# Performance work log

Measured on AMD Instinct MI355X. Metric: run time of the kernel, lower is better.

## Reference

```python
import jax, jax.numpy as jnp
import numpy as np

D_MODEL = 1024
NUM_HEADS = 16
HEAD_SIZE = D_MODEL // NUM_HEADS
ROPE_BASE = 10000.0
RMS_EPS = 1e-6


def rms_norm(x, scale):
    # torchtune RMSNorm: fp32 compute, eps=1e-6, learned scale
    xf = x.astype(jnp.float32)
    n = xf * jax.lax.rsqrt(jnp.mean(xf * xf, axis=-1, keepdims=True) + RMS_EPS)
    return (n * scale).astype(x.dtype)


def rope(x):
    # torchtune RotaryPositionalEmbeddings: interleaved pairs. x: [B,T,H,hd]
    B, T, H, hd = x.shape
    half = hd // 2
    theta = 1.0 / (ROPE_BASE ** (jnp.arange(0, hd, 2, dtype=jnp.float32) / hd))  # [half]
    ang = jnp.arange(T, dtype=jnp.float32)[:, None] * theta[None, :]  # [T,half]
    cos = jnp.cos(ang)[None, :, None, :]  # [1,T,1,half]
    sin = jnp.sin(ang)[None, :, None, :]
    xs = x.reshape(B, T, H, half, 2)
    x0, x1 = xs[..., 0], xs[..., 1]
    out = jnp.stack([x0 * cos - x1 * sin, x1 * cos + x0 * sin], axis=-1)
    return out.reshape(B, T, H, hd).astype(x.dtype)


def setup_inputs() -> dict:
    key = jax.random.key(0)
    ks = jax.random.split(key, 10)
    s = 0.02
    D = D_MODEL
    return {
        "x": jax.random.normal(ks[0], (2, 2048, D), dtype=jnp.float32),
        "rms_scale": jnp.ones((D,), dtype=jnp.float32),
        "in_proj_w": jax.random.normal(ks[1], (3 * D, D), dtype=jnp.float32) * s,
        "in_proj_b": jnp.zeros((3 * D,), dtype=jnp.float32),
        "out_proj_w": jax.random.normal(ks[2], (D, D), dtype=jnp.float32) * s,
        "out_proj_b": jnp.zeros((D,), dtype=jnp.float32),
        "w1": jax.random.normal(ks[3], (4 * D, D), dtype=jnp.float32) * s,
        "b1": jnp.zeros((4 * D,), dtype=jnp.float32),
        "w2": jax.random.normal(ks[4], (D, 4 * D), dtype=jnp.float32) * s,
        "b2": jnp.zeros((D,), dtype=jnp.float32),
    }


def reference(x, rms_scale, in_proj_w, in_proj_b, out_proj_w, out_proj_b, w1, b1, w2, b2):
    B, T, D = x.shape
    H, hd = NUM_HEADS, HEAD_SIZE

    xn = rms_norm(x, rms_scale)
    # RoPE on pre-projection q/k (as in original module), value = xn
    q_in = rope(xn.reshape(B, T, H, hd)).reshape(B, T, D)
    k_in = rope(xn.reshape(B, T, H, hd)).reshape(B, T, D)
    v_in = xn

    Wq, Wk, Wv = jnp.split(in_proj_w, 3, axis=0)
    bq, bk, bv = jnp.split(in_proj_b, 3, axis=0)
    q = (q_in @ Wq.T + bq).reshape(B, T, H, hd).transpose(0, 2, 1, 3)  # [B,H,T,hd]
    k = (k_in @ Wk.T + bk).reshape(B, T, H, hd).transpose(0, 2, 1, 3)
    v = (v_in @ Wv.T + bv).reshape(B, T, H, hd).transpose(0, 2, 1, 3)

    scores = jnp.einsum('bhqd,bhkd->bhqk', q, k) / jnp.sqrt(jnp.float32(hd))
    causal = jnp.tril(jnp.ones((T, T), dtype=bool))  # True = keep
    scores = jnp.where(causal[None, None], scores, jnp.float32(-1e30))
    attn = jax.nn.softmax(scores, axis=-1)
    ctx = jnp.einsum('bhqk,bhkd->bhqd', attn, v)  # [B,H,T,hd]
    attn_out = ctx.transpose(0, 2, 1, 3).reshape(B, T, D) @ out_proj_w.T + out_proj_b

    # NOTE: original overwrites x with attention output (no residual on attention)
    y = attn_out
    yn = rms_norm(y, rms_scale)
    ffn = jax.nn.silu(yn @ w1.T + b1) @ w2.T + b2
    return y + ffn
```

## Files before the change

kernel.cpp:

```cpp
#include <hip/hip_runtime.h>
#include <math.h>
#include <stdint.h>

#define D_MODEL 1024
#define NUM_HEADS 16
#define HEAD_SIZE 64
#define SEQ_T 2048

typedef __bf16 bf16;
typedef __bf16 bf16x8 __attribute__((ext_vector_type(8)));
typedef float f32x4 __attribute__((ext_vector_type(4)));

__device__ __forceinline__ void gld_lds16(const bf16* g, bf16* l) {
    __builtin_amdgcn_global_load_lds(
        (__attribute__((address_space(1))) void*)(const_cast<bf16*>(g)),
        (__attribute__((address_space(3))) void*)(l), 16, 0, 0);
}

struct __align__(8) b4pack { bf16 v[4]; };

__global__ __launch_bounds__(256) void cast_all_weights(const float* __restrict__ s0, bf16* __restrict__ d0, int n0,
                                                        const float* __restrict__ s1, bf16* __restrict__ d1, int n1,
                                                        const float* __restrict__ s2, bf16* __restrict__ d2, int n2,
                                                        const float* __restrict__ s3, bf16* __restrict__ d3, int n3) {
    int i = (blockIdx.x * 256 + threadIdx.x) * 4;
    const float* src;
    bf16* dst;
    if (i < n0) { src = s0; dst = d0; }
    else if (i < n0 + n1) { i -= n0; src = s1; dst = d1; }
    else if (i < n0 + n1 + n2) { i -= n0 + n1; src = s2; dst = d2; }
    else { i -= n0 + n1 + n2; if (i >= n3) return; src = s3; dst = d3; }
    float4 v = *(const float4*)(src + i);
    b4pack o;
    o.v[0] = (bf16)v.x; o.v[1] = (bf16)v.y; o.v[2] = (bf16)v.z; o.v[3] = (bf16)v.w;
    *(b4pack*)(dst + i) = o;
}

__global__ __launch_bounds__(256) void rmsnorm_rope_kernel(const float* __restrict__ x,
                                                           const float* __restrict__ scale,
                                                           bf16* __restrict__ xn,
                                                           bf16* __restrict__ rp, int T) {
    __shared__ float red[4];
    int row = blockIdx.x;
    int t = row % T;
    const float* xp = x + (size_t)row * D_MODEL;
    int tid = threadIdx.x;
    float4 xv = *(const float4*)(xp + tid * 4);
    float s = xv.x * xv.x + xv.y * xv.y + xv.z * xv.z + xv.w * xv.w;
    for (int off = 32; off; off >>= 1) s += __shfl_down(s, off);
    if ((tid & 63) == 0) red[tid >> 6] = s;
    __syncthreads();
    if (tid == 0) red[0] = red[0] + red[1] + red[2] + red[3];
    __syncthreads();
    float inv = rsqrtf(red[0] * (1.0f / D_MODEL) + 1e-6f);
    float4 sc = *(const float4*)(scale + tid * 4);
    float n0 = xv.x * inv * sc.x, n1 = xv.y * inv * sc.y;
    float n2 = xv.z * inv * sc.z, n3 = xv.w * inv * sc.w;
    b4pack pn;
    pn.v[0] = (bf16)n0; pn.v[1] = (bf16)n1; pn.v[2] = (bf16)n2; pn.v[3] = (bf16)n3;
    *(b4pack*)(xn + (size_t)row * D_MODEL + tid * 4) = pn;
    int p0 = 2 * tid;
    float th0 = expf(-0.2878231366242557f * (float)(p0 & 31));
    float th1 = expf(-0.2878231366242557f * (float)((p0 + 1) & 31));
    float s0, c0, s1, c1;
    sincosf((float)t * th0, &s0, &c0);
    sincosf((float)t * th1, &s1, &c1);
    b4pack pr;
    pr.v[0] = (bf16)(n0 * c0 - n1 * s0);
    pr.v[1] = (bf16)(n1 * c0 + n0 * s0);
    pr.v[2] = (bf16)(n2 * c1 - n3 * s1);
    pr.v[3] = (bf16)(n3 * c1 + n2 * s1);
    *(b4pack*)(rp + (size_t)row * D_MODEL + tid * 4) = pr;
}

__global__ __launch_bounds__(256) void rmsnorm_kernel(const float* __restrict__ x,
                                                      const float* __restrict__ scale,
                                                      bf16* __restrict__ out) {
    __shared__ float red[4];
    int row = blockIdx.x;
    const float* xp = x + (size_t)row * D_MODEL;
    bf16* op = out + (size_t)row * D_MODEL;
    int tid = threadIdx.x;
    float s = 0.f;
    for (int i = tid; i < D_MODEL; i += 256) { float v = xp[i]; s += v * v; }
    for (int off = 32; off; off >>= 1) s += __shfl_down(s, off);
    if ((tid & 63) == 0) red[tid >> 6] = s;
    __syncthreads();
    if (tid == 0) red[0] = red[0] + red[1] + red[2] + red[3];
    __syncthreads();
    float inv = rsqrtf(red[0] * (1.0f / D_MODEL) + 1e-6f);
    for (int i = tid; i < D_MODEL; i += 256) op[i] = (bf16)(xp[i] * inv * scale[i]);
}

template <int ACT, int ADD, int OUT_BF16, int VT>
__global__ __launch_bounds__(256) void gemm_bf16(const bf16* __restrict__ A,
                                                 const bf16* __restrict__ A2, int splitN,
                                                 const bf16* __restrict__ W,
                                                 const float* __restrict__ bias,
                                                 float* __restrict__ Cf,
                                                 bf16* __restrict__ Cb,
                                                 bf16* __restrict__ Vtp, int Tlen,
                                                 int M, int N, int K) {
    __shared__ __align__(16) bf16 As[128 * 32];
    __shared__ __align__(16) bf16 Bs[128 * 32];
    int tid = threadIdx.x;
    int m0 = blockIdx.y * 128, n0 = blockIdx.x * 128;
    const bf16* Ag = (n0 < splitN) ? A : A2;

    int lane = tid & 63, w = tid >> 6;
    int wm = w >> 1, wn = w & 1;
    int lm = lane & 15, quad = lane >> 4;

    int c0 = tid, c1 = tid + 256;
    int ar0 = c0 >> 2, ak0 = (c0 & 3) * 8;
    int ar1 = c1 >> 2, ak1 = (c1 & 3) * 8;

    f32x4 acc[4][4];
#pragma unroll
    for (int i = 0; i < 4; i++)
#pragma unroll
        for (int j = 0; j < 4; j++)
#pragma unroll
            for (int r = 0; r < 4; r++) acc[i][j][r] = 0.f;

    int abase = (wm * 64 + lm) * 32 + quad * 8;
    int bbase = (wn * 64 + lm) * 32 + quad * 8;

    for (int k0 = 0; k0 < K; k0 += 32) {
        __syncthreads();
        gld_lds16(Ag + (size_t)(m0 + ar0) * K + k0 + ak0, As + c0 * 8);
        gld_lds16(Ag + (size_t)(m0 + ar1) * K + k0 + ak1, As + c1 * 8);
        gld_lds16(W  + (size_t)(n0 + ar0) * K + k0 + ak0, Bs + c0 * 8);
        gld_lds16(W  + (size_t)(n0 + ar1) * K + k0 + ak1, Bs + c1 * 8);
        __syncthreads();
        bf16x8 af[4], bfr[4];
#pragma unroll
        for (int i = 0; i < 4; i++) af[i] = *(const bf16x8*)&As[abase + i * 16 * 32];
#pragma unroll
        for (int j = 0; j < 4; j++) bfr[j] = *(const bf16x8*)&Bs[bbase + j * 16 * 32];
#pragma unroll
        for (int i = 0; i < 4; i++)
#pragma unroll
            for (int j = 0; j < 4; j++)
                acc[i][j] = __builtin_amdgcn_mfma_f32_16x16x32_bf16(af[i], bfr[j], acc[i][j], 0, 0, 0);
    }

    if (VT && n0 >= 2 * D_MODEL) {
#pragma unroll
        for (int j = 0; j < 4; j++) {
            int col = n0 + wn * 64 + j * 16 + lm;
            int dimg = col - 2 * D_MODEL;
            float bv = bias[col];
#pragma unroll
            for (int i = 0; i < 4; i++) {
                int row0 = m0 + wm * 64 + i * 16 + quad * 4;
                int bb = row0 / Tlen, t0 = row0 % Tlen;
                b4pack pk;
#pragma unroll
                for (int r = 0; r < 4; r++) pk.v[r] = (bf16)(acc[i][j][r] + bv);
                *(b4pack*)(Vtp + ((size_t)bb * D_MODEL + dimg) * Tlen + t0) = pk;
            }
        }
        return;
    }

#pragma unroll
    for (int j = 0; j < 4; j++) {
        int col = n0 + wn * 64 + j * 16 + lm;
        float bv = bias[col];
#pragma unroll
        for (int i = 0; i < 4; i++) {
#pragma unroll
            for (int r = 0; r < 4; r++) {
                int row = m0 + wm * 64 + i * 16 + quad * 4 + r;
                float v = acc[i][j][r] + bv;
                if (ACT == 1) v = v / (1.f + __expf(-v));
                size_t idx = (size_t)row * N + col;
                if (ADD) v += Cf[idx];
                if (OUT_BF16) Cb[idx] = (bf16)v;
                else Cf[idx] = v;
            }
        }
    }
}

template <int ADD>
__global__ __launch_bounds__(256) void gemm_bf16_skinny2(const bf16* __restrict__ A,
                                                         const bf16* __restrict__ W,
                                                         const float* __restrict__ bias,
                                                         float* __restrict__ Cf,
                                                         int M, int N, int K) {
    __shared__ __align__(16) bf16 As[2][64 * 64];
    __shared__ __align__(16) bf16 Bs[2][128 * 64];
    int tid = threadIdx.x;

    int nblk = gridDim.x;
    int q = nblk >> 3;
    int swz = (blockIdx.x & 7) * q + (blockIdx.x >> 3);
    int nb = swz & 7;
    int mb = swz >> 3;
    int m0 = mb * 64, n0 = nb * 128;

    int lane = tid & 63, w = tid >> 6;
    int wm = w >> 1, wn = w & 1;
    int lm = lane & 15, quad = lane >> 4;
    int lm7 = lm & 7;

    int ar0 = tid >> 3, ac0 = (tid & 7) ^ (ar0 & 7);
    int t1 = tid + 256;
    int ar1 = t1 >> 3, ac1 = (t1 & 7) ^ (ar1 & 7);

    f32x4 acc[2][4];
#pragma unroll
    for (int i = 0; i < 2; i++)
#pragma unroll
        for (int j = 0; j < 4; j++)
#pragma unroll
            for (int r = 0; r < 4; r++) acc[i][j][r] = 0.f;

    int nt = K >> 6;

    {
        gld_lds16(A + (size_t)(m0 + ar0) * K + ac0 * 8, &As[0][0] + tid * 8);
        gld_lds16(A + (size_t)(m0 + ar1) * K + ac1 * 8, &As[0][0] + t1 * 8);
#pragma unroll
        for (int i = 0; i < 4; i++) {
            int c = tid + 256 * i;
            int r = c >> 3, cc = (c & 7) ^ (r & 7);
            gld_lds16(W + (size_t)(n0 + r) * K + cc * 8, &Bs[0][0] + c * 8);
        }
    }

    for (int t = 0; t < nt; ++t) {
        int cur = t & 1;
        if (t + 1 < nt) {
            int k0 = (t + 1) << 6;
            bf16* as = &As[cur ^ 1][0];
            bf16* bs = &Bs[cur ^ 1][0];
            gld_lds16(A + (size_t)(m0 + ar0) * K + k0 + ac0 * 8, as + tid * 8);
            gld_lds16(A + (size_t)(m0 + ar1) * K + k0 + ac1 * 8, as + t1 * 8);
#pragma unroll
            for (int i = 0; i < 4; i++) {
                int c = tid + 256 * i;
                int r = c >> 3, cc = (c & 7) ^ (r & 7);
                gld_lds16(W + (size_t)(n0 + r) * K + k0 + cc * 8, bs + c * 8);
            }
            asm volatile("s_waitcnt vmcnt(6)" ::: "memory");
        } else {
            asm volatile("s_waitcnt vmcnt(0)" ::: "memory");
        }
        __builtin_amdgcn_s_barrier();

        const bf16* as = &As[cur][0];
        const bf16* bs = &Bs[cur][0];
        bf16x8 af[2][2], bfr[4][2];
#pragma unroll
        for (int i = 0; i < 2; i++) {
            int row = wm * 32 + i * 16 + lm;
#pragma unroll
            for (int h = 0; h < 2; h++)
                af[i][h] = *(const bf16x8*)&as[row * 64 + ((h * 4 + quad) ^ lm7) * 8];
        }
#pragma unroll
        for (int j = 0; j < 4; j++) {
            int row = wn * 64 + j * 16 + lm;
#pragma unroll
            for (int h = 0; h < 2; h++)
                bfr[j][h] = *(const bf16x8*)&bs[row * 64 + ((h * 4 + quad) ^ lm7) * 8];
        }
#pragma unroll
        for (int i = 0; i < 2; i++)
#pragma unroll
            for (int j = 0; j < 4; j++) {
                acc[i][j] = __builtin_amdgcn_mfma_f32_16x16x32_bf16(af[i][0], bfr[j][0], acc[i][j], 0, 0, 0);
                acc[i][j] = __builtin_amdgcn_mfma_f32_16x16x32_bf16(af[i][1], bfr[j][1], acc[i][j], 0, 0, 0);
            }
        asm volatile("" ::: "memory");
        __builtin_amdgcn_s_barrier();
    }

#pragma unroll
    for (int j = 0; j < 4; j++) {
        int col = n0 + wn * 64 + j * 16 + lm;
        float bv = bias[col];
#pragma unroll
        for (int i = 0; i < 2; i++) {
#pragma unroll
            for (int r = 0; r < 4; r++) {
                int row = m0 + wm * 32 + i * 16 + quad * 4 + r;
                float v = acc[i][j][r] + bv;
                size_t idx = (size_t)row * N + col;
                if (ADD) v += Cf[idx];
                Cf[idx] = v;
            }
        }
    }
}

__global__ __launch_bounds__(256) void attn_mfma_kernel(const bf16* __restrict__ QKV,
                                                        const bf16* __restrict__ Vt,
                                                        bf16* __restrict__ Og, int T) {
    __shared__ __align__(16) bf16 Ks0[64 * 64];
    __shared__ __align__(16) bf16 Ks1[64 * 64];
    __shared__ __align__(16) bf16 Vs0[64 * 64];
    __shared__ __align__(16) bf16 Vs1[64 * 64];
    __shared__ __align__(16) bf16 Ps[4 * 16 * 64];
    const int ldq = 3 * D_MODEL;
    int bidx = blockIdx.x;
    int c = bidx & 7;
    int rest = bidx >> 3;
    int r4 = rest >> 5;
    int w5 = rest & 31;
    int bhoct = w5 >> 3;
    int tslot = w5 & 7;
    int bh = bhoct * 8 + c;
    int qt = (r4 & 1) ? (24 - 8 * r4 + tslot) : (31 - 8 * r4 - tslot);
    int h = bh & (NUM_HEADS - 1), b = bh / NUM_HEADS;
    int tid = threadIdx.x;
    int w = tid >> 6, lane = tid & 63;
    int lm = lane & 15, quad = lane >> 4;
    int q0 = qt * 64, qrow0 = q0 + w * 16;

    int s0 = tid, s1 = tid + 256;
    int sr0 = s0 >> 3, sc0 = (s0 & 7) ^ (sr0 & 7);
    int sr1 = s1 >> 3, sc1 = (s1 & 7) ^ (sr1 & 7);

    const bf16* Qp = QKV + ((size_t)(b * T + qrow0 + lm)) * ldq + h * HEAD_SIZE + quad * 8;
    bf16x8 qf0 = *(const bf16x8*)Qp;
    bf16x8 qf1 = *(const bf16x8*)(Qp + 32);

    const bf16* Kbase = QKV + ((size_t)b * T) * ldq + D_MODEL + h * HEAD_SIZE;
    const bf16* Vbase = Vt + ((size_t)b * D_MODEL + h * HEAD_SIZE) * T;
    const float C = 0.1803368801111204f;
    bf16* PsW = Ps + w * 16 * 64;
    int lm7 = lm & 7;

    f32x4 o[4];
    float m_i[4], l_i[4];
#pragma unroll
    for (int r = 0; r < 4; r++) {
        m_i[r] = -3.0e38f;
        l_i[r] = 0.f;
        o[r] = (f32x4){0.f, 0.f, 0.f, 0.f};
    }

    int nkt2 = (qt + 2) >> 1;
    for (int kt = 0; kt < nkt2; kt++) {
        int k0 = kt * 128;
        __syncthreads();
        gld_lds16(Kbase + (size_t)(k0 + sr0) * ldq + sc0 * 8, Ks0 + s0 * 8);
        gld_lds16(Kbase + (size_t)(k0 + sr1) * ldq + sc1 * 8, Ks0 + s1 * 8);
        gld_lds16(Kbase + (size_t)(k0 + 64 + sr0) * ldq + sc0 * 8, Ks1 + s0 * 8);
        gld_lds16(Kbase + (size_t)(k0 + 64 + sr1) * ldq + sc1 * 8, Ks1 + s1 * 8);
        gld_lds16(Vbase + (size_t)sr0 * T + k0 + sc0 * 8, Vs0 + s0 * 8);
        gld_lds16(Vbase + (size_t)sr1 * T + k0 + sc1 * 8, Vs0 + s1 * 8);
        gld_lds16(Vbase + (size_t)sr0 * T + k0 + 64 + sc0 * 8, Vs1 + s0 * 8);
        gld_lds16(Vbase + (size_t)sr1 * T + k0 + 64 + sc1 * 8, Vs1 + s1 * 8);
        __syncthreads();

        f32x4 sa[2][4];
#pragma unroll
        for (int u = 0; u < 2; u++) {
            const bf16* Ksu = u ? Ks1 : Ks0;
#pragma unroll
            for (int jb = 0; jb < 4; jb++) {
                int n = jb * 16 + lm;
                bf16x8 kf0 = *(const bf16x8*)&Ksu[(n * 8 + (quad ^ lm7)) * 8];
                bf16x8 kf1 = *(const bf16x8*)&Ksu[(n * 8 + ((quad + 4) ^ lm7)) * 8];
                f32x4 a = {0.f, 0.f, 0.f, 0.f};
                a = __builtin_amdgcn_mfma_f32_16x16x32_bf16(qf0, kf0, a, 0, 0, 0);
                a = __builtin_amdgcn_mfma_f32_16x16x32_bf16(qf1, kf1, a, 0, 0, 0);
                sa[u][jb] = a;
            }
        }
        if (kt == nkt2 - 1) {
#pragma unroll
            for (int u = 0; u < 2; u++)
#pragma unroll
                for (int jb = 0; jb < 4; jb++)
#pragma unroll
                    for (int r = 0; r < 4; r++)
                        if (k0 + u * 64 + jb * 16 + lm > qrow0 + quad * 4 + r)
                            sa[u][jb][r] = -3.0e38f;
        }
#pragma unroll
        for (int r = 0; r < 4; r++) {
            float mn = fmaxf(fmaxf(sa[0][0][r], sa[0][1][r]), fmaxf(sa[0][2][r], sa[0][3][r]));
            mn = fmaxf(mn, fmaxf(fmaxf(sa[1][0][r], sa[1][1][r]), fmaxf(sa[1][2][r], sa[1][3][r])));
            mn = fmaxf(mn, __shfl_xor(mn, 1));
            mn = fmaxf(mn, __shfl_xor(mn, 2));
            mn = fmaxf(mn, __shfl_xor(mn, 4));
            mn = fmaxf(mn, __shfl_xor(mn, 8));
            float mt = fmaxf(m_i[r], mn);
            float alpha = exp2f((m_i[r] - mt) * C);
            m_i[r] = mt;
            float nb2 = -mt * C;
            float rs = 0.f;
#pragma unroll
            for (int u = 0; u < 2; u++)
#pragma unroll
                for (int jb = 0; jb < 4; jb++) {
                    float p = exp2f(fmaf(sa[u][jb][r], C, nb2));
                    sa[u][jb][r] = p;
                    rs += p;
                }
            rs += __shfl_xor(rs, 1);
            rs += __shfl_xor(rs, 2);
            rs += __shfl_xor(rs, 4);
            rs += __shfl_xor(rs, 8);
            l_i[r] = l_i[r] * alpha + rs;
#pragma unroll
            for (int db = 0; db < 4; db++) o[db][r] *= alpha;
        }
#pragma unroll
        for (int u = 0; u < 2; u++) {
            const bf16* Vsu = u ? Vs1 : Vs0;
#pragma unroll
            for (int jb = 0; jb < 4; jb++) {
                int g = jb * 2 + (lm >> 3);
#pragma unroll
                for (int r = 0; r < 4; r++) {
                    int row = quad * 4 + r;
                    PsW[row * 64 + ((g ^ (row & 7)) * 8) + lm7] = (bf16)sa[u][jb][r];
                }
            }
            bf16x8 pf0 = *(const bf16x8*)&PsW[lm * 64 + ((quad ^ lm7) * 8)];
            bf16x8 pf1 = *(const bf16x8*)&PsW[lm * 64 + (((quad + 4) ^ lm7) * 8)];
#pragma unroll
            for (int db = 0; db < 4; db++) {
                int n = db * 16 + lm;
                bf16x8 vf0 = *(const bf16x8*)&Vsu[(n * 8 + (quad ^ lm7)) * 8];
                bf16x8 vf1 = *(const bf16x8*)&Vsu[(n * 8 + ((quad + 4) ^ lm7)) * 8];
                o[db] = __builtin_amdgcn_mfma_f32_16x16x32_bf16(pf0, vf0, o[db], 0, 0, 0);
                o[db] = __builtin_amdgcn_mfma_f32_16x16x32_bf16(pf1, vf1, o[db], 0, 0, 0);
            }
        }
    }

    float inv[4];
#pragma unroll
    for (int r = 0; r < 4; r++) inv[r] = 1.f / l_i[r];
    bf16* Ob = Og + ((size_t)(b * T + qrow0 + quad * 4)) * D_MODEL + h * HEAD_SIZE + lm;
#pragma unroll
    for (int r = 0; r < 4; r++)
#pragma unroll
        for (int db = 0; db < 4; db++)
            Ob[(size_t)r * D_MODEL + db * 16] = (bf16)(o[db][r] * inv[r]);
}

extern "C" void kernel_launch(void* const* d_in, const int* in_sizes, int n_in,
                              void* d_out, int out_size, void* d_ws, size_t ws_size,
                              hipStream_t stream) {
    const float* x          = (const float*)d_in[0];
    const float* rms_scale  = (const float*)d_in[1];
    const float* in_proj_w  = (const float*)d_in[2];
    const float* in_proj_b  = (const float*)d_in[3];
    const float* out_proj_w = (const float*)d_in[4];
    const float* out_proj_b = (const float*)d_in[5];
    const float* w1         = (const float*)d_in[6];
    const float* b1         = (const float*)d_in[7];
    const float* w2         = (const float*)d_in[8];
    const float* b2         = (const float*)d_in[9];
    float* out = (float*)d_out;

    const int rows = in_sizes[0] / D_MODEL;
    const int T = SEQ_T;
    const int B = rows / T;
    const int D = D_MODEL;

    bf16* inwb  = (bf16*)d_ws;
    bf16* outwb = inwb + (size_t)3 * D * D;
    bf16* w1b   = outwb + (size_t)D * D;
    bf16* w2b   = w1b + (size_t)4 * D * D;
    bf16* XNb   = w2b + (size_t)4 * D * D;
    bf16* RPb   = XNb + (size_t)rows * D;
    bf16* QKV   = RPb + (size_t)rows * D;
    bf16* Vt    = QKV + (size_t)rows * 3 * D;
    bf16* CTXb  = XNb;
    bf16* YNb   = RPb;
    bf16* H1b   = QKV;

    {
        int n0 = 3 * D * D, n1 = D * D, n2 = 4 * D * D, n3 = 4 * D * D;
        int tot4 = (n0 + n1 + n2 + n3) / 4;
        cast_all_weights<<<(tot4 + 255) / 256, 256, 0, stream>>>(
            in_proj_w, inwb, n0, out_proj_w, outwb, n1, w1, w1b, n2, w2, w2b, n3);
    }
    rmsnorm_rope_kernel<<<rows, 256, 0, stream>>>(x, rms_scale, XNb, RPb, T);
    {
        dim3 g(3 * D / 128, rows / 128);
        gemm_bf16<0, 0, 1, 1><<<g, 256, 0, stream>>>(RPb, XNb, 2 * D, inwb, in_proj_b,
                                                     nullptr, QKV, Vt, T, rows, 3 * D, D);
    }
    attn_mfma_kernel<<<B * NUM_HEADS * (T / 64), 256, 0, stream>>>(QKV, Vt, CTXb, T);
    {
        int nblk = (D / 128) * (rows / 64);
        gemm_bf16_skinny2<0><<<nblk, 256, 0, stream>>>(CTXb, outwb, out_proj_b, out,
                                                       rows, D, D);
    }
    rmsnorm_kernel<<<rows, 256, 0, stream>>>(out, rms_scale, YNb);
    {
        dim3 g(4 * D / 128, rows / 128);
        gemm_bf16<1, 0, 1, 0><<<g, 256, 0, stream>>>(YNb, YNb, 4 * D, w1b, b1,
                                                     nullptr, H1b, nullptr, 1, rows, 4 * D, D);
    }
    {
        int nblk = (D / 128) * (rows / 64);
        gemm_bf16_skinny2<1><<<nblk, 256, 0, stream>>>(H1b, w2b, b2, out,
                                                       rows, D, 4 * D);
    }
}
```

Baseline: 382.3 us.

## Pair complementary causal query tiles per block with double-buffered K/V staging

Each attention block now processes two query tiles (31-p and p) so every block does the same causal work, and the two tiles share each K/V tile loaded into LDS. K/V staging is double-buffered with explicit vmcnt waits so the next tile's loads overlap compute, and MFMA sections are wrapped in s_setprio. The grid halves and LDS per block doubles, with launch bounds set for two blocks per CU, which can reduce occupancy and parallelism.

```diff
diff --git a/kernel.cpp b/kernel.cpp
--- a/kernel.cpp
+++ b/kernel.cpp
@@ -297,37 +297,36 @@
     }
 }
 
-__global__ __launch_bounds__(256) void attn_mfma_kernel(const bf16* __restrict__ QKV,
-                                                        const bf16* __restrict__ Vt,
-                                                        bf16* __restrict__ Og, int T) {
-    __shared__ __align__(16) bf16 Ks0[64 * 64];
-    __shared__ __align__(16) bf16 Ks1[64 * 64];
-    __shared__ __align__(16) bf16 Vs0[64 * 64];
-    __shared__ __align__(16) bf16 Vs1[64 * 64];
+__global__ __launch_bounds__(256, 2) void attn_mfma_kernel(const bf16* __restrict__ QKV,
+                                                           const bf16* __restrict__ Vt,
+                                                           bf16* __restrict__ Og, int T) {
+    __shared__ __align__(16) bf16 Ks[2][2][64 * 64];
+    __shared__ __align__(16) bf16 Vs[2][2][64 * 64];
     __shared__ __align__(16) bf16 Ps[4 * 16 * 64];
     const int ldq = 3 * D_MODEL;
     int bidx = blockIdx.x;
     int c = bidx & 7;
     int rest = bidx >> 3;
-    int r4 = rest >> 5;
-    int w5 = rest & 31;
-    int bhoct = w5 >> 3;
-    int tslot = w5 & 7;
+    int p = rest & 15;
+    int bhoct = rest >> 4;
     int bh = bhoct * 8 + c;
-    int qt = (r4 & 1) ? (24 - 8 * r4 + tslot) : (31 - 8 * r4 - tslot);
+    int qtA = 31 - p, qtB = p;
     int h = bh & (NUM_HEADS - 1), b = bh / NUM_HEADS;
     int tid = threadIdx.x;
     int w = tid >> 6, lane = tid & 63;
     int lm = lane & 15, quad = lane >> 4;
-    int q0 = qt * 64, qrow0 = q0 + w * 16;
+    int qrowA = qtA * 64 + w * 16, qrowB = qtB * 64 + w * 16;
 
     int s0 = tid, s1 = tid + 256;
     int sr0 = s0 >> 3, sc0 = (s0 & 7) ^ (sr0 & 7);
     int sr1 = s1 >> 3, sc1 = (s1 & 7) ^ (sr1 & 7);
 
-    const bf16* Qp = QKV + ((size_t)(b * T + qrow0 + lm)) * ldq + h * HEAD_SIZE + quad * 8;
-    bf16x8 qf0 = *(const bf16x8*)Qp;
-    bf16x8 qf1 = *(const bf16x8*)(Qp + 32);
+    const bf16* QpA = QKV + ((size_t)(b * T + qrowA + lm)) * ldq + h * HEAD_SIZE + quad * 8;
+    bf16x8 qfA0 = *(const bf16x8*)QpA;
+    bf16x8 qfA1 = *(const bf16x8*)(QpA + 32);
+    const bf16* QpB = QKV + ((size_t)(b * T + qrowB + lm)) * ldq + h * HEAD_SIZE + quad * 8;
+    bf16x8 qfB0 = *(const bf16x8*)QpB;
+    bf16x8 qfB1 = *(const bf16x8*)(QpB + 32);
 
     const bf16* Kbase = QKV + ((size_t)b * T) * ldq + D_MODEL + h * HEAD_SIZE;
     const bf16* Vbase = Vt + ((size_t)b * D_MODEL + h * HEAD_SIZE) * T;
@@ -335,33 +334,35 @@
     bf16* PsW = Ps + w * 16 * 64;
     int lm7 = lm & 7;
 
-    f32x4 o[4];
-    float m_i[4], l_i[4];
+    f32x4 oA[4], oB[4];
+    float mA[4], lA[4], mB[4], lB[4];
 #pragma unroll
     for (int r = 0; r < 4; r++) {
-        m_i[r] = -3.0e38f;
-        l_i[r] = 0.f;
-        o[r] = (f32x4){0.f, 0.f, 0.f, 0.f};
-    }
-
-    int nkt2 = (qt + 2) >> 1;
-    for (int kt = 0; kt < nkt2; kt++) {
-        int k0 = kt * 128;
-        __syncthreads();
-        gld_lds16(Kbase + (size_t)(k0 + sr0) * ldq + sc0 * 8, Ks0 + s0 * 8);
-        gld_lds16(Kbase + (size_t)(k0 + sr1) * ldq + sc1 * 8, Ks0 + s1 * 8);
-        gld_lds16(Kbase + (size_t)(k0 + 64 + sr0) * ldq + sc0 * 8, Ks1 + s0 * 8);
-        gld_lds16(Kbase + (size_t)(k0 + 64 + sr1) * ldq + sc1 * 8, Ks1 + s1 * 8);
-        gld_lds16(Vbase + (size_t)sr0 * T + k0 + sc0 * 8, Vs0 + s0 * 8);
-        gld_lds16(Vbase + (size_t)sr1 * T + k0 + sc1 * 8, Vs0 + s1 * 8);
-        gld_lds16(Vbase + (size_t)sr0 * T + k0 + 64 + sc0 * 8, Vs1 + s0 * 8);
-        gld_lds16(Vbase + (size_t)sr1 * T + k0 + 64 + sc1 * 8, Vs1 + s1 * 8);
-        __syncthreads();
-
+        mA[r] = -3.0e38f; lA[r] = 0.f; oA[r] = (f32x4){0.f, 0.f, 0.f, 0.f};
+        mB[r] = -3.0e38f; lB[r] = 0.f; oB[r] = (f32x4){0.f, 0.f, 0.f, 0.f};
+    }
+
+    int nktA = (qtA + 2) >> 1;
+    int nktB = (qtB + 2) >> 1;
+
+    auto stage = [&](int buf, int k0) {
+        gld_lds16(Kbase + (size_t)(k0 + sr0) * ldq + sc0 * 8, &Ks[buf][0][0] + s0 * 8);
+        gld_lds16(Kbase + (size_t)(k0 + sr1) * ldq + sc1 * 8, &Ks[buf][0][0] + s1 * 8);
+        gld_lds16(Kbase + (size_t)(k0 + 64 + sr0) * ldq + sc0 * 8, &Ks[buf][1][0] + s0 * 8);
+        gld_lds16(Kbase + (size_t)(k0 + 64 + sr1) * ldq + sc1 * 8, &Ks[buf][1][0] + s1 * 8);
+        gld_lds16(Vbase + (size_t)sr0 * T + k0 + sc0 * 8, &Vs[buf][0][0] + s0 * 8);
+        gld_lds16(Vbase + (size_t)sr1 * T + k0 + sc1 * 8, &Vs[buf][0][0] + s1 * 8);
+        gld_lds16(Vbase + (size_t)sr0 * T + k0 + 64 + sc0 * 8, &Vs[buf][1][0] + s0 * 8);
+        gld_lds16(Vbase + (size_t)sr1 * T + k0 + 64 + sc1 * 8, &Vs[buf][1][0] + s1 * 8);
+    };
+
+    auto run_tile = [&](int cur, int k0, bf16x8 qf0, bf16x8 qf1, int qrow0,
+                        f32x4 (&o)[4], float (&m_i)[4], float (&l_i)[4], bool lastmask) {
         f32x4 sa[2][4];
+        __builtin_amdgcn_s_setprio(1);
 #pragma unroll
         for (int u = 0; u < 2; u++) {
-            const bf16* Ksu = u ? Ks1 : Ks0;
+            const bf16* Ksu = &Ks[cur][u][0];
 #pragma unroll
             for (int jb = 0; jb < 4; jb++) {
                 int n = jb * 16 + lm;
@@ -373,7 +374,8 @@
                 sa[u][jb] = a;
             }
         }
-        if (kt == nkt2 - 1) {
+        __builtin_amdgcn_s_setprio(0);
+        if (lastmask) {
 #pragma unroll
             for (int u = 0; u < 2; u++)
 #pragma unroll
@@ -400,9 +402,9 @@
             for (int u = 0; u < 2; u++)
 #pragma unroll
                 for (int jb = 0; jb < 4; jb++) {
-                    float p = exp2f(fmaf(sa[u][jb][r], C, nb2));
-                    sa[u][jb][r] = p;
-                    rs += p;
+                    float pv = exp2f(fmaf(sa[u][jb][r], C, nb2));
+                    sa[u][jb][r] = pv;
+                    rs += pv;
                 }
             rs += __shfl_xor(rs, 1);
             rs += __shfl_xor(rs, 2);
@@ -414,7 +416,7 @@
         }
 #pragma unroll
         for (int u = 0; u < 2; u++) {
-            const bf16* Vsu = u ? Vs1 : Vs0;
+            const bf16* Vsu = &Vs[cur][u][0];
 #pragma unroll
             for (int jb = 0; jb < 4; jb++) {
                 int g = jb * 2 + (lm >> 3);
@@ -426,6 +428,7 @@
             }
             bf16x8 pf0 = *(const bf16x8*)&PsW[lm * 64 + ((quad ^ lm7) * 8)];
             bf16x8 pf1 = *(const bf16x8*)&PsW[lm * 64 + (((quad + 4) ^ lm7) * 8)];
+            __builtin_amdgcn_s_setprio(1);
 #pragma unroll
             for (int db = 0; db < 4; db++) {
                 int n = db * 16 + lm;
@@ -434,18 +437,51 @@
                 o[db] = __builtin_amdgcn_mfma_f32_16x16x32_bf16(pf0, vf0, o[db], 0, 0, 0);
                 o[db] = __builtin_amdgcn_mfma_f32_16x16x32_bf16(pf1, vf1, o[db], 0, 0, 0);
             }
-        }
-    }
-
-    float inv[4];
-#pragma unroll
-    for (int r = 0; r < 4; r++) inv[r] = 1.f / l_i[r];
-    bf16* Ob = Og + ((size_t)(b * T + qrow0 + quad * 4)) * D_MODEL + h * HEAD_SIZE + lm;
-#pragma unroll
-    for (int r = 0; r < 4; r++)
-#pragma unroll
-        for (int db = 0; db < 4; db++)
-            Ob[(size_t)r * D_MODEL + db * 16] = (bf16)(o[db][r] * inv[r]);
+            __builtin_amdgcn_s_setprio(0);
+        }
+    };
+
+    stage(0, 0);
+    for (int kt = 0; kt < nktA; kt++) {
+        int cur = kt & 1;
+        if (kt + 1 < nktA) {
+            stage(cur ^ 1, (kt + 1) * 128);
+            asm volatile("s_waitcnt vmcnt(8)" ::: "memory");
+        } else {
+            asm volatile("s_waitcnt vmcnt(0)" ::: "memory");
+        }
+        __builtin_amdgcn_s_barrier();
+        asm volatile("" ::: "memory");
+        int k0 = kt * 128;
+        run_tile(cur, k0, qfA0, qfA1, qrowA, oA, mA, lA, kt == nktA - 1);
+        if (kt < nktB)
+            run_tile(cur, k0, qfB0, qfB1, qrowB, oB, mB, lB, kt == nktB - 1);
+        asm volatile("" ::: "memory");
+        __builtin_amdgcn_s_barrier();
+    }
+
+    {
+        float inv[4];
+#pragma unroll
+        for (int r = 0; r < 4; r++) inv[r] = 1.f / lA[r];
+        bf16* Ob = Og + ((size_t)(b * T + qrowA + quad * 4)) * D_MODEL + h * HEAD_SIZE + lm;
+#pragma unroll
+        for (int r = 0; r < 4; r++)
+#pragma unroll
+            for (int db = 0; db < 4; db++)
+                Ob[(size_t)r * D_MODEL + db * 16] = (bf16)(oA[db][r] * inv[r]);
+    }
+    {
+        float inv[4];
+#pragma unroll
+        for (int r = 0; r < 4; r++) inv[r] = 1.f / lB[r];
+        bf16* Ob = Og + ((size_t)(b * T + qrowB + quad * 4)) * D_MODEL + h * HEAD_SIZE + lm;
+#pragma unroll
+        for (int r = 0; r < 4; r++)
+#pragma unroll
+            for (int db = 0; db < 4; db++)
+                Ob[(size_t)r * D_MODEL + db * 16] = (bf16)(oB[db][r] * inv[r]);
+    }
 }
 
 extern "C" void kernel_launch(void* const* d_in, const int* in_sizes, int n_in,
@@ -492,7 +528,7 @@
         gemm_bf16<0, 0, 1, 1><<<g, 256, 0, stream>>>(RPb, XNb, 2 * D, inwb, in_proj_b,
                                                      nullptr, QKV, Vt, T, rows, 3 * D, D);
     }
-    attn_mfma_kernel<<<B * NUM_HEADS * (T / 64), 256, 0, stream>>>(QKV, Vt, CTXb, T);
+    attn_mfma_kernel<<<B * NUM_HEADS * (T / 128), 256, 0, stream>>>(QKV, Vt, CTXb, T);
     {
         int nblk = (D / 128) * (rows / 64);
         gemm_bf16_skinny2<0><<<nblk, 256, 0, stream>>>(CTXb, outwb, out_proj_b, out,
```

Result: no change. 378.6 us (-1.0%).
